# Performance work log

Hardware: AMD Instinct MI355X
Metric: run time of the kernel (lower is better)

## Reference

```python
import jax, jax.numpy as jnp
import numpy as np

N_HEAD = 16
HEAD_DIM = 64
EPS = 1e-5
ROPE_BASE = 10000.0


def setup_inputs() -> dict:
    key = jax.random.key(0)
    ks = jax.random.split(key, 3)
    B, T, C = 4, 2048, 1024
    x = jax.random.normal(ks[0], (B, T, C), dtype=jnp.float32)
    Wqkv = jax.random.normal(ks[1], (C, 3 * C), dtype=jnp.float32) * (C ** -0.5)
    Wproj = jax.random.normal(ks[2], (C, C), dtype=jnp.float32) * (C ** -0.5)
    q_norm_w = jnp.ones((HEAD_DIM,), dtype=jnp.float32)
    k_norm_w = jnp.ones((HEAD_DIM,), dtype=jnp.float32)
    return {"x": x, "Wqkv": Wqkv, "Wproj": Wproj, "q_norm_w": q_norm_w, "k_norm_w": k_norm_w}


def _rms_norm(x, w):
    xf = x.astype(jnp.float32)
    normed = xf * jax.lax.rsqrt(jnp.mean(xf * xf, axis=-1, keepdims=True) + EPS)
    return (normed * w).astype(x.dtype)


def _rope_tables(T, dtype):
    inv_freq = 1.0 / (ROPE_BASE ** (jnp.arange(0, HEAD_DIM, 2, dtype=jnp.float32) / HEAD_DIM))
    t = jnp.arange(T, dtype=jnp.float32)
    freqs = jnp.outer(t, inv_freq)              # [T, D/2]
    emb = jnp.concatenate([freqs, freqs], -1)   # [T, D]
    return jnp.cos(emb).astype(dtype), jnp.sin(emb).astype(dtype)


def _rotate_half(x):
    x1, x2 = jnp.split(x, 2, axis=-1)
    return jnp.concatenate([-x2, x1], axis=-1)


def reference(x, Wqkv, Wproj, q_norm_w, k_norm_w):
    B, T, C = x.shape
    qkv = x @ Wqkv                               # [B, T, 3C]
    q, k, v = jnp.split(qkv, 3, axis=-1)
    # [B, H, T, D]
    q = q.reshape(B, T, N_HEAD, HEAD_DIM).transpose(0, 2, 1, 3)
    k = k.reshape(B, T, N_HEAD, HEAD_DIM).transpose(0, 2, 1, 3)
    v = v.reshape(B, T, N_HEAD, HEAD_DIM).transpose(0, 2, 1, 3)
    # per-head QK RMSNorm
    q = _rms_norm(q, q_norm_w)
    k = _rms_norm(k, k_norm_w)
    # RoPE
    cos, sin = _rope_tables(T, q.dtype)          # [T, D] broadcast over B,H
    q = q * cos + _rotate_half(q) * sin
    k = k * cos + _rotate_half(k) * sin
    # causal attention
    scale = 1.0 / np.sqrt(HEAD_DIM)
    att = jnp.einsum('bhqd,bhkd->bhqk', q, k) * scale
    causal = jnp.tril(jnp.ones((T, T), dtype=bool))
    att = jnp.where(causal, att, -jnp.inf)
    att = jax.nn.softmax(att, axis=-1)
    y = jnp.einsum('bhqk,bhkd->bhqd', att, v)    # [B, H, T, D]
    y = y.transpose(0, 2, 1, 3).reshape(B, T, C)
    return y @ Wproj
```

## Files before the change

### kernel.cpp

```cpp
#include <hip/hip_runtime.h>
#include <cstdint>
#include <type_traits>

typedef __attribute__((ext_vector_type(8))) short bf16x8;
typedef __attribute__((ext_vector_type(4))) float f32x4;

typedef unsigned int __attribute__((address_space(1))) as1_uint;
typedef unsigned int __attribute__((address_space(3))) as3_uint;

__device__ __forceinline__ void llds16(const void* g, void* l) {
  __builtin_amdgcn_global_load_lds((const as1_uint*)g, (as3_uint*)l, 16, 0, 0);
}

__device__ __forceinline__ unsigned short f2bf(float f) {
  unsigned int u = __builtin_bit_cast(unsigned int, f);
  u = (u + 0x7fffu + ((u >> 16) & 1u)) >> 16;
  return (unsigned short)u;
}
__device__ __forceinline__ float bf2f(unsigned short h) {
  unsigned int u = ((unsigned int)h) << 16;
  return __builtin_bit_cast(float, u);
}

__global__ __launch_bounds__(256) void cvt_f32_bf16(const float* __restrict__ in,
                                                    unsigned short* __restrict__ out, int n4) {
  int i = blockIdx.x * blockDim.x + threadIdx.x;
  int stride = gridDim.x * blockDim.x;
  for (; i < n4; i += stride) {
    float4 v = ((const float4*)in)[i];
    uint2 p;
    p.x = (unsigned)f2bf(v.x) | ((unsigned)f2bf(v.y) << 16);
    p.y = (unsigned)f2bf(v.z) | ((unsigned)f2bf(v.w) << 16);
    ((uint2*)out)[i] = p;
  }
}

__global__ __launch_bounds__(256) void transpose_f32_bf16(const float* __restrict__ W,
                                                          unsigned short* __restrict__ Wt,
                                                          int K, int N) {
  __shared__ float tile[64][65];
  int n0 = blockIdx.x * 64, k0 = blockIdx.y * 64;
  int t = threadIdx.x;
  int lr = t >> 4, lc = (t & 15) * 4;
#pragma unroll
  for (int i = 0; i < 4; ++i) {
    int k = lr + i * 16;
    float4 v = *(const float4*)&W[(size_t)(k0 + k) * N + n0 + lc];
    tile[k][lc] = v.x; tile[k][lc + 1] = v.y; tile[k][lc + 2] = v.z; tile[k][lc + 3] = v.w;
  }
  __syncthreads();
  int n = t >> 2, kc = (t & 3) * 16;
  unsigned short* dst = &Wt[(size_t)(n0 + n) * K + k0 + kc];
#pragma unroll
  for (int j = 0; j < 16; ++j) dst[j] = f2bf(tile[kc + j][n]);
}

__global__ __launch_bounds__(256) void rope_tab(float* __restrict__ cosT, float* __restrict__ sinT) {
  int i = blockIdx.x * 256 + threadIdx.x;
  int t = i >> 5, j = i & 31;
  float inv = powf(10000.0f, -(float)j * (1.0f / 32.0f));
  float a = (float)t * inv;
  cosT[i] = cosf(a);
  sinT[i] = sinf(a);
}

template <typename OutT>
__global__ __launch_bounds__(256) void gemm_ring(const unsigned short* __restrict__ A,
                                                 const unsigned short* __restrict__ Bt,
                                                 OutT* __restrict__ C, int M, int N, int K) {
  __shared__ unsigned short As[3][128 * 32];
  __shared__ unsigned short Bs[3][128 * 32];
  const int tid = threadIdx.x;
  const int w = tid >> 6, lane = tid & 63;
  const int l15 = lane & 15, lg = lane >> 4;
  const int wr = w >> 1, wc = w & 1;

  const int nwg = gridDim.x * gridDim.y;
  const int lin = blockIdx.y * gridDim.x + blockIdx.x;
  const int swzb = (lin & 7) * (nwg >> 3) + (lin >> 3);
  const int bx = swzb % gridDim.x, by = swzb / gridDim.x;
  const int m0 = by * 128, n0 = bx * 128;

  const size_t K2 = (size_t)K * 2;
  const char* Ag = (const char*)A;
  const char* Bg = (const char*)Bt;

  const int rc = lane >> 2;
  const int cb = (lane & 3) * 16;

  auto stage = [&](int buf, int kt) {
#pragma unroll
    for (int i = 0; i < 2; ++i) {
      int c = w + i * 4;
      int row = c * 16 + rc;
      int srcc = cb ^ (((row >> 1) & 3) << 4);
      size_t kofs = (size_t)kt * 64 + srcc;
      llds16(Ag + (size_t)(m0 + row) * K2 + kofs, (char*)&As[buf][0] + c * 1024);
      llds16(Bg + (size_t)(n0 + row) * K2 + kofs, (char*)&Bs[buf][0] + c * 1024);
    }
  };

  f32x4 acc[4][4] = {};
  const int nk = K >> 5;

  stage(0, 0);
  stage(1, 1);

  int cur = 0;
  for (int t = 0; t < nk; ++t) {
    asm volatile("s_waitcnt vmcnt(4)" ::: "memory");
    __builtin_amdgcn_s_barrier();
    asm volatile("" ::: "memory");
    if (t + 2 < nk) stage(cur + 2 >= 3 ? cur - 1 : cur + 2, t + 2);

    const unsigned short* Ab = &As[cur][0];
    const unsigned short* Bb = &Bs[cur][0];
    bf16x8 af[4], bfr[4];
#pragma unroll
    for (int m = 0; m < 4; ++m) {
      int row = wr * 64 + m * 16 + l15;
      af[m] = *(const bf16x8*)((const char*)Ab + row * 64 + ((lg * 16) ^ (((row >> 1) & 3) << 4)));
    }
#pragma unroll
    for (int n = 0; n < 4; ++n) {
      int row = wc * 64 + n * 16 + l15;
      bfr[n] = *(const bf16x8*)((const char*)Bb + row * 64 + ((lg * 16) ^ (((row >> 1) & 3) << 4)));
    }
#pragma unroll
    for (int m = 0; m < 4; ++m)
#pragma unroll
      for (int n = 0; n < 4; ++n)
        acc[m][n] = __builtin_amdgcn_mfma_f32_16x16x32_bf16(af[m], bfr[n], acc[m][n], 0, 0, 0);

    cur = (cur == 2) ? 0 : cur + 1;
  }

#pragma unroll
  for (int m = 0; m < 4; ++m)
#pragma unroll
    for (int n = 0; n < 4; ++n) {
      int row = m0 + wr * 64 + m * 16 + lg * 4;
      int col = n0 + wc * 64 + n * 16 + l15;
#pragma unroll
      for (int r = 0; r < 4; ++r) {
        if constexpr (std::is_same<OutT, float>::value)
          C[(size_t)(row + r) * N + col] = acc[m][n][r];
        else
          C[(size_t)(row + r) * N + col] = f2bf(acc[m][n][r]);
      }
    }
}

__global__ __launch_bounds__(256) void qkv_post(const unsigned short* __restrict__ qkv,
                                                const float* __restrict__ qw,
                                                const float* __restrict__ kw,
                                                const float* __restrict__ cosT,
                                                const float* __restrict__ sinT,
                                                unsigned short* __restrict__ Qr,
                                                unsigned short* __restrict__ Kr) {
  int bt = blockIdx.x;
  int b = bt >> 11, t = bt & 2047;
  int tid = threadIdx.x, h = tid >> 4, g = tid & 15, d0 = g * 4;
  const unsigned short* base = qkv + (size_t)bt * 3072;
  int dm = d0 & 31;
  float4 cv = *(const float4*)&cosT[t * 32 + dm];
  float4 sv = *(const float4*)&sinT[t * 32 + dm];
  float sgn = (g < 8) ? -1.0f : 1.0f;
  size_t oofs = (((size_t)(b * 16 + h)) * 2048 + t) * 64 + d0;

#pragma unroll
  for (int s = 0; s < 2; ++s) {
    const float* wt = s ? kw : qw;
    float scale = s ? 1.0f : 0.18033688011112042f;
    unsigned short* outp = s ? Kr : Qr;
    ushort4 raw = *(const ushort4*)(base + s * 1024 + h * 64 + d0);
    float x0 = bf2f(raw.x), x1 = bf2f(raw.y), x2 = bf2f(raw.z), x3 = bf2f(raw.w);
    float ssq = x0 * x0 + x1 * x1 + x2 * x2 + x3 * x3;
    ssq += __shfl_xor(ssq, 1); ssq += __shfl_xor(ssq, 2);
    ssq += __shfl_xor(ssq, 4); ssq += __shfl_xor(ssq, 8);
    float f = rsqrtf(ssq * (1.0f / 64.0f) + 1e-5f);
    float4 w4 = *(const float4*)&wt[d0];
    float n0 = x0 * f * w4.x, n1 = x1 * f * w4.y, n2 = x2 * f * w4.z, n3 = x3 * f * w4.w;
    float p0 = __shfl_xor(n0, 8), p1 = __shfl_xor(n1, 8), p2 = __shfl_xor(n2, 8), p3 = __shfl_xor(n3, 8);
    float o0 = (n0 * cv.x + sgn * p0 * sv.x) * scale;
    float o1 = (n1 * cv.y + sgn * p1 * sv.y) * scale;
    float o2 = (n2 * cv.z + sgn * p2 * sv.z) * scale;
    float o3 = (n3 * cv.w + sgn * p3 * sv.w) * scale;
    uint2 pk;
    pk.x = (unsigned)f2bf(o0) | ((unsigned)f2bf(o1) << 16);
    pk.y = (unsigned)f2bf(o2) | ((unsigned)f2bf(o3) << 16);
    *(uint2*)(outp + oofs) = pk;
  }
}

__global__ __launch_bounds__(256) void vtrans(const unsigned short* __restrict__ qkv,
                                              unsigned short* __restrict__ Vtg) {
  __shared__ unsigned short tile[64][72];
  int bh = blockIdx.y, b = bh >> 4, h = bh & 15;
  int t0 = blockIdx.x * 64;
  int tid = threadIdx.x;
  int r = tid >> 2, c0 = (tid & 3) * 16;
  const unsigned short* src = qkv + (size_t)(b * 2048 + t0 + r) * 3072 + 2048 + h * 64 + c0;
  *(bf16x8*)&tile[r][c0] = *(const bf16x8*)src;
  *(bf16x8*)&tile[r][c0 + 8] = *(const bf16x8*)(src + 8);
  __syncthreads();
  int d = tid >> 2, t4 = (tid & 3) * 16;
  unsigned short* dst = &Vtg[((size_t)bh * 64 + d) * 2048 + t0 + t4];
  unsigned short pack[16];
#pragma unroll
  for (int j = 0; j < 16; ++j) pack[j] = tile[t4 + j][d];
  *(bf16x8*)dst = *(bf16x8*)&pack[0];
  *(bf16x8*)(dst + 8) = *(bf16x8*)&pack[8];
}

__global__ __launch_bounds__(256) void attn_fwd(const unsigned short* __restrict__ Q,
                                                const unsigned short* __restrict__ K,
                                                const unsigned short* __restrict__ Vtg,
                                                unsigned short* __restrict__ Y) {
  const int bh = blockIdx.x;
  const int pr = blockIdx.y;
  const int b = bh >> 4, h = bh & 15;
  const int tid = threadIdx.x;
  const int w = tid >> 6, lane = tid & 63;
  const int l15 = lane & 15, lg = lane >> 4;

  __shared__ unsigned short Kl[2][64 * 64];
  __shared__ unsigned short Vt[2][64 * 64];
  __shared__ unsigned short Pl[4][16 * 64];

  const size_t bhT = (size_t)bh * 2048;
  const char* Kg = (const char*)(K + bhT * 64);
  const char* Vg = (const char*)(Vtg + bhT * 64);

  auto stage = [&](int buf, int kt) {
#pragma unroll
    for (int i = 0; i < 2; ++i) {
      int c = w * 2 + i;
      int pos = c * 1024 + lane * 16;
      int row = pos >> 7, cb = pos & 127;
      int srcb = cb ^ ((row & 7) << 4);
      llds16(Kg + ((size_t)(kt * 64 + row)) * 128 + srcb,
             (char*)&Kl[buf][0] + c * 1024);
      llds16(Vg + (size_t)row * 4096 + (size_t)kt * 128 + srcb,
             (char*)&Vt[buf][0] + c * 1024);
    }
  };

  auto run_qtile = [&](int qtb) {
    const int qbase = qtb * 64;
    const unsigned short* Qp = Q + (bhT + qbase + w * 16 + l15) * 64 + lg * 8;
    bf16x8 aq[2];
    aq[0] = *(const bf16x8*)(Qp);
    aq[1] = *(const bf16x8*)(Qp + 32);

    f32x4 o[4] = {};
    float psum = 0.0f;

    char* Pw = (char*)&Pl[w][0];
    const int psw = (l15 & 7) << 4;

    for (int kt = 0; kt <= qtb; ++kt) {
      const int cur = kt & 1;
      if (kt < qtb) stage(cur ^ 1, kt + 1);
      const char* Kc = (const char*)&Kl[cur][0];
      const char* Vc = (const char*)&Vt[cur][0];

      f32x4 s[4] = {};
      __builtin_amdgcn_s_setprio(1);
#pragma unroll
      for (int n = 0; n < 4; ++n) {
        int r = n * 16 + l15, sw = (r & 7) << 4;
#pragma unroll
        for (int ks = 0; ks < 2; ++ks) {
          bf16x8 bk = *(const bf16x8*)(Kc + r * 128 + ((ks * 64 + lg * 16) ^ sw));
          s[n] = __builtin_amdgcn_mfma_f32_16x16x32_bf16(bk, aq[ks], s[n], 0, 0, 0);
        }
      }
      __builtin_amdgcn_s_setprio(0);

      if (kt == qtb) {
#pragma unroll
        for (int n = 0; n < 4; ++n)
#pragma unroll
          for (int r = 0; r < 4; ++r)
            if (n * 16 + lg * 4 + r > w * 16 + l15) s[n][r] = -1e30f;
      }

#pragma unroll
      for (int n = 0; n < 4; ++n) {
        float p0 = __builtin_exp2f(s[n][0]);
        float p1 = __builtin_exp2f(s[n][1]);
        float p2 = __builtin_exp2f(s[n][2]);
        float p3 = __builtin_exp2f(s[n][3]);
        psum += (p0 + p1) + (p2 + p3);
        uint2 pk;
        pk.x = ((__builtin_bit_cast(unsigned int, p0) + 0x8000u) >> 16) |
               (((__builtin_bit_cast(unsigned int, p1) + 0x8000u) >> 16) << 16);
        pk.y = ((__builtin_bit_cast(unsigned int, p2) + 0x8000u) >> 16) |
               (((__builtin_bit_cast(unsigned int, p3) + 0x8000u) >> 16) << 16);
        *(uint2*)(Pw + l15 * 128 + ((n * 32 + lg * 8) ^ psw)) = pk;
      }
      asm volatile("" ::: "memory");

      bf16x8 ap[2];
      ap[0] = *(const bf16x8*)(Pw + l15 * 128 + ((lg * 16) ^ psw));
      ap[1] = *(const bf16x8*)(Pw + l15 * 128 + ((64 + lg * 16) ^ psw));

      __builtin_amdgcn_s_setprio(1);
#pragma unroll
      for (int df = 0; df < 4; ++df) {
        int rr = df * 16 + l15, sw = (rr & 7) << 4;
#pragma unroll
        for (int ks = 0; ks < 2; ++ks) {
          bf16x8 bv = *(const bf16x8*)(Vc + rr * 128 + ((ks * 64 + lg * 16) ^ sw));
          o[df] = __builtin_amdgcn_mfma_f32_16x16x32_bf16(bv, ap[ks], o[df], 0, 0, 0);
        }
      }
      __builtin_amdgcn_s_setprio(0);
      __syncthreads();
    }

    psum += __shfl_xor(psum, 16);
    psum += __shfl_xor(psum, 32);
    float inv = 1.0f / psum;

    size_t q = qbase + w * 16 + l15;
    unsigned short* yp = Y + ((size_t)b * 2048 + q) * 1024 + h * 64 + lg * 4;
#pragma unroll
    for (int df = 0; df < 4; ++df) {
      ushort4 v;
      v.x = f2bf(o[df][0] * inv);
      v.y = f2bf(o[df][1] * inv);
      v.z = f2bf(o[df][2] * inv);
      v.w = f2bf(o[df][3] * inv);
      *(ushort4*)(yp + df * 16) = v;
    }
  };

  stage(0, 0);
  __syncthreads();
  run_qtile(31 - pr);
  stage(0, 0);
  __syncthreads();
  run_qtile(pr);
}

extern "C" void kernel_launch(void* const* d_in, const int* in_sizes, int n_in,
                              void* d_out, int out_size, void* d_ws, size_t ws_size,
                              hipStream_t stream) {
  const float* x = (const float*)d_in[0];
  const float* Wqkv = (const float*)d_in[1];
  const float* Wproj = (const float*)d_in[2];
  const float* qw = (const float*)d_in[3];
  const float* kw = (const float*)d_in[4];
  float* out = (float*)d_out;

  char* ws = (char*)d_ws;
  unsigned short* xb = (unsigned short*)ws;        ws += (size_t)8192 * 1024 * 2;
  unsigned short* wqkvt = (unsigned short*)ws;     ws += (size_t)3072 * 1024 * 2;
  unsigned short* wprojt = (unsigned short*)ws;    ws += (size_t)1024 * 1024 * 2;
  unsigned short* qkvb = (unsigned short*)ws;      ws += (size_t)8192 * 3072 * 2;
  unsigned short* Qr = (unsigned short*)ws;        ws += (size_t)64 * 2048 * 64 * 2;
  unsigned short* Kr = (unsigned short*)ws;        ws += (size_t)64 * 2048 * 64 * 2;
  unsigned short* Vtg = (unsigned short*)ws;       ws += (size_t)64 * 64 * 2048 * 2;
  unsigned short* yb = (unsigned short*)ws;        ws += (size_t)8192 * 1024 * 2;
  float* cosT = (float*)ws;                        ws += (size_t)2048 * 32 * 4;
  float* sinT = (float*)ws;                        ws += (size_t)2048 * 32 * 4;

  cvt_f32_bf16<<<2048, 256, 0, stream>>>(x, xb, 8192 * 1024 / 4);
  transpose_f32_bf16<<<dim3(48, 16), 256, 0, stream>>>(Wqkv, wqkvt, 1024, 3072);
  transpose_f32_bf16<<<dim3(16, 16), 256, 0, stream>>>(Wproj, wprojt, 1024, 1024);
  rope_tab<<<256, 256, 0, stream>>>(cosT, sinT);
  gemm_ring<unsigned short><<<dim3(24, 64), 256, 0, stream>>>(xb, wqkvt, qkvb, 8192, 3072, 1024);
  qkv_post<<<8192, 256, 0, stream>>>(qkvb, qw, kw, cosT, sinT, Qr, Kr);
  vtrans<<<dim3(32, 64), 256, 0, stream>>>(qkvb, Vtg);
  attn_fwd<<<dim3(64, 16), 256, 0, stream>>>(Qr, Kr, Vtg, yb);
  gemm_ring<float><<<dim3(8, 64), 256, 0, stream>>>(yb, wprojt, out, 8192, 1024, 1024);
}
```

Before: 208.9 us.

## Fuse QK RMSNorm, RoPE and V transpose into the QKV GEMM epilogue

The QKV projection GEMM now applies per-head RMSNorm, RoPE and the Q scale directly on its accumulators and writes Q/K in head-major layout. It also transposes V through shared memory into the Vt layout, so the intermediate qkv buffer and the separate qkv_post and vtrans kernels go away. The RoPE table is stored transposed so the epilogue can read cos/sin contiguously along time. The GEMM's final iteration now waits for all loads to finish. The aim is to avoid a 48MB round trip and two kernel launches, at the cost of a heavier epilogue with scattered 2-byte stores for Q/K.

```diff
diff --git a/kernel.cpp b/kernel.cpp
--- a/kernel.cpp
+++ b/kernel.cpp
@@ -55,10 +55,10 @@
   for (int j = 0; j < 16; ++j) dst[j] = f2bf(tile[kc + j][n]);
 }
 
-__global__ __launch_bounds__(256) void rope_tab(float* __restrict__ cosT, float* __restrict__ sinT) {
+__global__ __launch_bounds__(256) void rope_tabT(float* __restrict__ cosT, float* __restrict__ sinT) {
   int i = blockIdx.x * 256 + threadIdx.x;
-  int t = i >> 5, j = i & 31;
-  float inv = powf(10000.0f, -(float)j * (1.0f / 32.0f));
+  int dm = i >> 11, t = i & 2047;
+  float inv = powf(10000.0f, -(float)dm * (1.0f / 32.0f));
   float a = (float)t * inv;
   cosT[i] = cosf(a);
   sinT[i] = sinf(a);
@@ -84,7 +84,6 @@
   const size_t K2 = (size_t)K * 2;
   const char* Ag = (const char*)A;
   const char* Bg = (const char*)Bt;
-
   const int rc = lane >> 2;
   const int cb = (lane & 3) * 16;
 
@@ -102,13 +101,12 @@
 
   f32x4 acc[4][4] = {};
   const int nk = K >> 5;
-
   stage(0, 0);
   stage(1, 1);
-
   int cur = 0;
   for (int t = 0; t < nk; ++t) {
-    asm volatile("s_waitcnt vmcnt(4)" ::: "memory");
+    if (t + 1 < nk) asm volatile("s_waitcnt vmcnt(4)" ::: "memory");
+    else            asm volatile("s_waitcnt vmcnt(0)" ::: "memory");
     __builtin_amdgcn_s_barrier();
     asm volatile("" ::: "memory");
     if (t + 2 < nk) stage(cur + 2 >= 3 ? cur - 1 : cur + 2, t + 2);
@@ -131,7 +129,6 @@
 #pragma unroll
       for (int n = 0; n < 4; ++n)
         acc[m][n] = __builtin_amdgcn_mfma_f32_16x16x32_bf16(af[m], bfr[n], acc[m][n], 0, 0, 0);
-
     cur = (cur == 2) ? 0 : cur + 1;
   }
 
@@ -151,66 +148,154 @@
     }
 }
 
-__global__ __launch_bounds__(256) void qkv_post(const unsigned short* __restrict__ qkv,
+__global__ __launch_bounds__(256) void gemm_qkv(const unsigned short* __restrict__ A,
+                                                const unsigned short* __restrict__ Bt,
                                                 const float* __restrict__ qw,
                                                 const float* __restrict__ kw,
-                                                const float* __restrict__ cosT,
-                                                const float* __restrict__ sinT,
+                                                const float* __restrict__ cosTT,
+                                                const float* __restrict__ sinTT,
                                                 unsigned short* __restrict__ Qr,
-                                                unsigned short* __restrict__ Kr) {
-  int bt = blockIdx.x;
-  int b = bt >> 11, t = bt & 2047;
-  int tid = threadIdx.x, h = tid >> 4, g = tid & 15, d0 = g * 4;
-  const unsigned short* base = qkv + (size_t)bt * 3072;
-  int dm = d0 & 31;
-  float4 cv = *(const float4*)&cosT[t * 32 + dm];
-  float4 sv = *(const float4*)&sinT[t * 32 + dm];
-  float sgn = (g < 8) ? -1.0f : 1.0f;
-  size_t oofs = (((size_t)(b * 16 + h)) * 2048 + t) * 64 + d0;
-
-#pragma unroll
-  for (int s = 0; s < 2; ++s) {
-    const float* wt = s ? kw : qw;
-    float scale = s ? 1.0f : 0.18033688011112042f;
-    unsigned short* outp = s ? Kr : Qr;
-    ushort4 raw = *(const ushort4*)(base + s * 1024 + h * 64 + d0);
-    float x0 = bf2f(raw.x), x1 = bf2f(raw.y), x2 = bf2f(raw.z), x3 = bf2f(raw.w);
-    float ssq = x0 * x0 + x1 * x1 + x2 * x2 + x3 * x3;
-    ssq += __shfl_xor(ssq, 1); ssq += __shfl_xor(ssq, 2);
-    ssq += __shfl_xor(ssq, 4); ssq += __shfl_xor(ssq, 8);
-    float f = rsqrtf(ssq * (1.0f / 64.0f) + 1e-5f);
-    float4 w4 = *(const float4*)&wt[d0];
-    float n0 = x0 * f * w4.x, n1 = x1 * f * w4.y, n2 = x2 * f * w4.z, n3 = x3 * f * w4.w;
-    float p0 = __shfl_xor(n0, 8), p1 = __shfl_xor(n1, 8), p2 = __shfl_xor(n2, 8), p3 = __shfl_xor(n3, 8);
-    float o0 = (n0 * cv.x + sgn * p0 * sv.x) * scale;
-    float o1 = (n1 * cv.y + sgn * p1 * sv.y) * scale;
-    float o2 = (n2 * cv.z + sgn * p2 * sv.z) * scale;
-    float o3 = (n3 * cv.w + sgn * p3 * sv.w) * scale;
-    uint2 pk;
-    pk.x = (unsigned)f2bf(o0) | ((unsigned)f2bf(o1) << 16);
-    pk.y = (unsigned)f2bf(o2) | ((unsigned)f2bf(o3) << 16);
-    *(uint2*)(outp + oofs) = pk;
+                                                unsigned short* __restrict__ Kr,
+                                                unsigned short* __restrict__ Vtg) {
+  constexpr int K = 1024;
+  __shared__ unsigned short smem[6 * 128 * 32];
+  unsigned short* As = smem;
+  unsigned short* Bs = smem + 3 * 128 * 32;
+
+  const int tid = threadIdx.x;
+  const int w = tid >> 6, lane = tid & 63;
+  const int l15 = lane & 15, lg = lane >> 4;
+  const int wr = w >> 1, wc = w & 1;
+
+  const int nwg = gridDim.x * gridDim.y;
+  const int lin = blockIdx.y * gridDim.x + blockIdx.x;
+  const int swzb = (lin & 7) * (nwg >> 3) + (lin >> 3);
+  const int bx = swzb % gridDim.x, by = swzb / gridDim.x;
+  const int m0 = by * 128, n0 = bx * 128;
+
+  const size_t K2 = (size_t)K * 2;
+  const char* Ag = (const char*)A;
+  const char* Bg = (const char*)Bt;
+  const int rc = lane >> 2;
+  const int cb = (lane & 3) * 16;
+
+  auto stage = [&](int buf, int kt) {
+#pragma unroll
+    for (int i = 0; i < 2; ++i) {
+      int c = w + i * 4;
+      int row = c * 16 + rc;
+      int srcc = cb ^ (((row >> 1) & 3) << 4);
+      size_t kofs = (size_t)kt * 64 + srcc;
+      llds16(Ag + (size_t)(m0 + row) * K2 + kofs, (char*)As + buf * 8192 + c * 1024);
+      llds16(Bg + (size_t)(n0 + row) * K2 + kofs, (char*)Bs + buf * 8192 + c * 1024);
+    }
+  };
+
+  f32x4 acc[4][4] = {};
+  const int nk = K >> 5;
+  stage(0, 0);
+  stage(1, 1);
+  int cur = 0;
+  for (int t = 0; t < nk; ++t) {
+    if (t + 1 < nk) asm volatile("s_waitcnt vmcnt(4)" ::: "memory");
+    else            asm volatile("s_waitcnt vmcnt(0)" ::: "memory");
+    __builtin_amdgcn_s_barrier();
+    asm volatile("" ::: "memory");
+    if (t + 2 < nk) stage(cur + 2 >= 3 ? cur - 1 : cur + 2, t + 2);
+
+    const char* Ab = (const char*)As + cur * 8192;
+    const char* Bb = (const char*)Bs + cur * 8192;
+    bf16x8 af[4], bfr[4];
+#pragma unroll
+    for (int m = 0; m < 4; ++m) {
+      int row = wr * 64 + m * 16 + l15;
+      af[m] = *(const bf16x8*)(Ab + row * 64 + ((lg * 16) ^ (((row >> 1) & 3) << 4)));
+    }
+#pragma unroll
+    for (int n = 0; n < 4; ++n) {
+      int row = wc * 64 + n * 16 + l15;
+      bfr[n] = *(const bf16x8*)(Bb + row * 64 + ((lg * 16) ^ (((row >> 1) & 3) << 4)));
+    }
+#pragma unroll
+    for (int m = 0; m < 4; ++m)
+#pragma unroll
+      for (int n = 0; n < 4; ++n)
+        acc[m][n] = __builtin_amdgcn_mfma_f32_16x16x32_bf16(af[m], bfr[n], acc[m][n], 0, 0, 0);
+    cur = (cur == 2) ? 0 : cur + 1;
   }
-}
-
-__global__ __launch_bounds__(256) void vtrans(const unsigned short* __restrict__ qkv,
-                                              unsigned short* __restrict__ Vtg) {
-  __shared__ unsigned short tile[64][72];
-  int bh = blockIdx.y, b = bh >> 4, h = bh & 15;
-  int t0 = blockIdx.x * 64;
-  int tid = threadIdx.x;
-  int r = tid >> 2, c0 = (tid & 3) * 16;
-  const unsigned short* src = qkv + (size_t)(b * 2048 + t0 + r) * 3072 + 2048 + h * 64 + c0;
-  *(bf16x8*)&tile[r][c0] = *(const bf16x8*)src;
-  *(bf16x8*)&tile[r][c0 + 8] = *(const bf16x8*)(src + 8);
-  __syncthreads();
-  int d = tid >> 2, t4 = (tid & 3) * 16;
-  unsigned short* dst = &Vtg[((size_t)bh * 64 + d) * 2048 + t0 + t4];
-  unsigned short pack[16];
-#pragma unroll
-  for (int j = 0; j < 16; ++j) pack[j] = tile[t4 + j][d];
-  *(bf16x8*)dst = *(bf16x8*)&pack[0];
-  *(bf16x8*)(dst + 8) = *(bf16x8*)&pack[8];
+
+  const int cls = bx >> 3;
+  const int head = (bx & 7) * 2 + wc;
+  const int rowb = m0 + wr * 64;
+  const int b = rowb >> 11;
+  const int tl = rowb & 2047;
+  const int bh = b * 16 + head;
+
+  if (cls < 2) {
+    const float* wt = cls ? kw : qw;
+    const float scale = cls ? 1.0f : 0.18033688011112042f;
+    unsigned short* outp = cls ? Kr : Qr;
+    float wv[4];
+#pragma unroll
+    for (int n = 0; n < 4; ++n) wv[n] = wt[n * 16 + l15];
+    const float* c0p = cosTT + l15 * 2048;
+    const float* c1p = cosTT + (16 + l15) * 2048;
+    const float* s0p = sinTT + l15 * 2048;
+    const float* s1p = sinTT + (16 + l15) * 2048;
+#pragma unroll
+    for (int m = 0; m < 4; ++m) {
+      int t0 = tl + m * 16 + lg * 4;
+      f32x4 ssq = {};
+#pragma unroll
+      for (int n = 0; n < 4; ++n) ssq += acc[m][n] * acc[m][n];
+#pragma unroll
+      for (int r = 0; r < 4; ++r) {
+        float v = ssq[r];
+        v += __shfl_xor(v, 1); v += __shfl_xor(v, 2);
+        v += __shfl_xor(v, 4); v += __shfl_xor(v, 8);
+        ssq[r] = rsqrtf(v * (1.0f / 64.0f) + 1e-5f) * scale;
+      }
+      f32x4 nv[4];
+#pragma unroll
+      for (int n = 0; n < 4; ++n) nv[n] = acc[m][n] * ssq * wv[n];
+      f32x4 cv0 = *(const f32x4*)(c0p + t0);
+      f32x4 cv1 = *(const f32x4*)(c1p + t0);
+      f32x4 sv0 = *(const f32x4*)(s0p + t0);
+      f32x4 sv1 = *(const f32x4*)(s1p + t0);
+      f32x4 ov[4];
+      ov[0] = nv[0] * cv0 - nv[2] * sv0;
+      ov[1] = nv[1] * cv1 - nv[3] * sv1;
+      ov[2] = nv[2] * cv0 + nv[0] * sv0;
+      ov[3] = nv[3] * cv1 + nv[1] * sv1;
+      unsigned short* yp = outp + ((size_t)bh * 2048 + t0) * 64 + l15;
+#pragma unroll
+      for (int n = 0; n < 4; ++n)
+#pragma unroll
+        for (int r = 0; r < 4; ++r)
+          yp[(size_t)r * 64 + n * 16] = f2bf(ov[n][r]);
+    }
+  } else {
+    __syncthreads();
+    unsigned short* tb = smem + w * (64 * 72);
+#pragma unroll
+    for (int m = 0; m < 4; ++m)
+#pragma unroll
+      for (int n = 0; n < 4; ++n) {
+        int d = n * 16 + l15, t = m * 16 + lg * 4;
+        ushort4 pk;
+        pk.x = f2bf(acc[m][n][0]); pk.y = f2bf(acc[m][n][1]);
+        pk.z = f2bf(acc[m][n][2]); pk.w = f2bf(acc[m][n][3]);
+        *(ushort4*)(tb + d * 72 + t) = pk;
+      }
+    asm volatile("" ::: "memory");
+    int d2 = lane;
+    unsigned short* vp = Vtg + ((size_t)bh * 64 + d2) * 2048 + tl;
+#pragma unroll
+    for (int j = 0; j < 8; ++j) {
+      bf16x8 vv = *(const bf16x8*)(tb + d2 * 72 + j * 8);
+      *(bf16x8*)(vp + j * 8) = vv;
+    }
+  }
 }
 
 __global__ __launch_bounds__(256) void attn_fwd(const unsigned short* __restrict__ Q,
@@ -359,21 +444,18 @@
   unsigned short* xb = (unsigned short*)ws;        ws += (size_t)8192 * 1024 * 2;
   unsigned short* wqkvt = (unsigned short*)ws;     ws += (size_t)3072 * 1024 * 2;
   unsigned short* wprojt = (unsigned short*)ws;    ws += (size_t)1024 * 1024 * 2;
-  unsigned short* qkvb = (unsigned short*)ws;      ws += (size_t)8192 * 3072 * 2;
   unsigned short* Qr = (unsigned short*)ws;        ws += (size_t)64 * 2048 * 64 * 2;
   unsigned short* Kr = (unsigned short*)ws;        ws += (size_t)64 * 2048 * 64 * 2;
   unsigned short* Vtg = (unsigned short*)ws;       ws += (size_t)64 * 64 * 2048 * 2;
   unsigned short* yb = (unsigned short*)ws;        ws += (size_t)8192 * 1024 * 2;
-  float* cosT = (float*)ws;                        ws += (size_t)2048 * 32 * 4;
-  float* sinT = (float*)ws;                        ws += (size_t)2048 * 32 * 4;
+  float* cosTT = (float*)ws;                       ws += (size_t)32 * 2048 * 4;
+  float* sinTT = (float*)ws;                       ws += (size_t)32 * 2048 * 4;
 
   cvt_f32_bf16<<<2048, 256, 0, stream>>>(x, xb, 8192 * 1024 / 4);
   transpose_f32_bf16<<<dim3(48, 16), 256, 0, stream>>>(Wqkv, wqkvt, 1024, 3072);
   transpose_f32_bf16<<<dim3(16, 16), 256, 0, stream>>>(Wproj, wprojt, 1024, 1024);
-  rope_tab<<<256, 256, 0, stream>>>(cosT, sinT);
-  gemm_ring<unsigned short><<<dim3(24, 64), 256, 0, stream>>>(xb, wqkvt, qkvb, 8192, 3072, 1024);
-  qkv_post<<<8192, 256, 0, stream>>>(qkvb, qw, kw, cosT, sinT, Qr, Kr);
-  vtrans<<<dim3(32, 64), 256, 0, stream>>>(qkvb, Vtg);
+  rope_tabT<<<256, 256, 0, stream>>>(cosTT, sinTT);
+  gemm_qkv<<<dim3(24, 64), 256, 0, stream>>>(xb, wqkvt, qw, kw, cosTT, sinTT, Qr, Kr, Vtg);
   attn_fwd<<<dim3(64, 16), 256, 0, stream>>>(Qr, Kr, Vtg, yb);
   gemm_ring<float><<<dim3(8, 64), 256, 0, stream>>>(yb, wprojt, out, 8192, 1024, 1024);
 }
```

Result: faster. 200.7 us (-3.9%).
